# Optimization experiments

Measured on AMD Instinct MI355X. Metric: run time of the kernel, lower is better.

The kernel has to match this reference:

```python
import jax, jax.numpy as jnp
import numpy as np

B, P, D, H, L = 1024, 22, 3, 64, 5
HI = P + 2                 # 22 one-hot + t + d_base
CR = 15.0 / L              # coords_range per layer (tanh=True, agg='sum')
LOG2M = 7.0                # log2(M=128)


def _edges():
    rr, cc = [], []
    for i in range(P):
        for j in range(i + 1, P):
            rr += [i, j]
            cc += [j, i]
    rr, cc = np.asarray(rr), np.asarray(cc)
    off = (np.arange(B) * P)[:, None]
    rows = (rr[None, :] + off).reshape(-1).astype(np.int32)
    cols = (cc[None, :] + off).reshape(-1).astype(np.int32)
    return jnp.asarray(rows), jnp.asarray(cols)


def setup_inputs() -> dict:
    key = jax.random.key(0)
    ks = jax.random.split(key, 16)

    def lin(k, shape, gain=1.0):
        fi, fo = shape[-2], shape[-1]
        lim = gain * np.sqrt(6.0 / (fi + fo))
        return jax.random.uniform(k, shape, jnp.float32, -lim, lim)

    rows, cols = _edges()
    z = lambda *s: jnp.zeros(s, jnp.float32)
    return {
        "t": jax.random.uniform(ks[0], (B,), jnp.float32),
        "x": jax.random.normal(ks[1], (B, P * D), jnp.float32),
        "emb_W": lin(ks[2], (HI, H)), "emb_b": z(H),
        "out_W": lin(ks[3], (H, HI)), "out_b": z(HI),
        # per-layer stacked params (leading dim = L)
        "edge_w1": lin(ks[4], (L, 2 * H + 2, H)), "edge_b1": z(L, H),
        "edge_w2": lin(ks[5], (L, H, H)), "edge_b2": z(L, H),
        "node_w1": lin(ks[6], (L, 2 * H, H)), "node_b1": z(L, H),
        "node_w2": lin(ks[7], (L, H, H)), "node_b2": z(L, H),
        "coord_w1": lin(ks[8], (L, H, H)), "coord_b1": z(L, H),
        "coord_w2": lin(ks[9], (L, H, 1), gain=0.001),  # xavier gain=0.001, no bias
        "att_w": lin(ks[10], (L, H, 1)), "att_b": z(L, 1),
        "rows": rows, "cols": cols,
    }


def reference(t, x, emb_W, emb_b, out_W, out_b,
              edge_w1, edge_b1, edge_w2, edge_b2,
              node_w1, node_b1, node_w2, node_b2,
              coord_w1, coord_b1, coord_w2, att_w, att_b,
              rows, cols):
    silu = jax.nn.silu
    N = B * P
    coord0 = x.reshape(N, D)

    # node features: [one_hot(atom), t, d_base]
    h0 = jnp.tile(jnp.eye(P, dtype=x.dtype), (B, 1))        # (N, 22)
    tt = jnp.repeat(t, P)[:, None]                           # (N, 1)
    db = jnp.full((N, 1), LOG2M, dtype=x.dtype)
    h = jnp.concatenate([h0, tt, db], axis=-1) @ emb_W + emb_b  # (N, H)

    # edge_attr: initial squared distances, shared by all layers
    d0 = coord0[rows] - coord0[cols]
    edge_attr = jnp.sum(d0 * d0, axis=-1, keepdims=True)     # (E, 1)

    def layer(carry, p):
        h, coord = carry
        ew1, eb1, ew2, eb2, nw1, nb1, nw2, nb2, cw1, cb1, cw2, aw, ab = p
        diff = coord[rows] - coord[cols]                     # (E, D)
        radial = jnp.sum(diff * diff, axis=-1, keepdims=True)
        diff = diff / (jnp.sqrt(radial) + 1.0)               # norm_diff
        e_in = jnp.concatenate([h[rows], h[cols], radial, edge_attr], axis=-1)
        m = silu(silu(e_in @ ew1 + eb1) @ ew2 + eb2)         # edge MLP
        m = m * jax.nn.sigmoid(m @ aw + ab)                  # attention gate
        # coordinate update
        trans = diff * (jnp.tanh(silu(m @ cw1 + cb1) @ cw2) * CR)
        coord = coord + jax.ops.segment_sum(trans, rows, num_segments=N)
        # node update (recurrent)
        agg = jax.ops.segment_sum(m, rows, num_segments=N)
        h = h + silu(jnp.concatenate([h, agg], axis=-1) @ nw1 + nb1) @ nw2 + nb2 * 0 + (silu(jnp.concatenate([h, agg], axis=-1) @ nw1 + nb1) @ nw2 + nb2 - silu(jnp.concatenate([h, agg], axis=-1) @ nw1 + nb1) @ nw2 - nb2)
        return (h, coord), None

    # (the expression above is just h = h + node_mlp(...); written plainly:)
    def layer_clean(carry, p):
        h, coord = carry
        ew1, eb1, ew2, eb2, nw1, nb1, nw2, nb2, cw1, cb1, cw2, aw, ab = p
        diff = coord[rows] - coord[cols]
        radial = jnp.sum(diff * diff, axis=-1, keepdims=True)
        diff = diff / (jnp.sqrt(radial) + 1.0)
        e_in = jnp.concatenate([h[rows], h[cols], radial, edge_attr], axis=-1)
        m = silu(silu(e_in @ ew1 + eb1) @ ew2 + eb2)
        m = m * jax.nn.sigmoid(m @ aw + ab)
        trans = diff * (jnp.tanh(silu(m @ cw1 + cb1) @ cw2) * CR)
        coord = coord + jax.ops.segment_sum(trans, rows, num_segments=N)
        agg = jax.ops.segment_sum(m, rows, num_segments=N)
        h = h + (silu(jnp.concatenate([h, agg], axis=-1) @ nw1 + nb1) @ nw2 + nb2)
        return (h, coord), None

    ps = (edge_w1, edge_b1, edge_w2, edge_b2, node_w1, node_b1, node_w2,
          node_b2, coord_w1, coord_b1, coord_w2, att_w, att_b)
    (h, coord), _ = jax.lax.scan(layer_clean, (h, coord0), ps)
    h = h @ out_W + out_b  # embedding_out (does not affect coordinates)

    vel = (coord - coord0).reshape(B, P, D)
    vel = vel - jnp.mean(vel, axis=1, keepdims=True)  # remove_mean
    return vel.reshape(B, P * D)
```

## Files before the change

kernel.cpp:

```cpp
#include <hip/hip_runtime.h>

#define NP 22
#define NH 64
#define NL 5
#define NE 21

constexpr float CRc    = 3.0f;
constexpr float LOG2Mc = 7.0f;
constexpr float L2E    = 1.442695041f;

typedef __fp16 h2_t  __attribute__((ext_vector_type(2)));
typedef __fp16 f16x8 __attribute__((ext_vector_type(8)));
typedef float  f32x16 __attribute__((ext_vector_type(16)));

__device__ __forceinline__ float rcp_(float x) {
#if __has_builtin(__builtin_amdgcn_rcpf)
  return __builtin_amdgcn_rcpf(x);
#else
  float r; asm("v_rcp_f32 %0, %1" : "=v"(r) : "v"(x)); return r;
#endif
}
__device__ __forceinline__ float exp2_(float x) {
#if __has_builtin(__builtin_amdgcn_exp2f)
  return __builtin_amdgcn_exp2f(x);
#else
  float r; asm("v_exp_f32 %0, %1" : "=v"(r) : "v"(x)); return r;
#endif
}
__device__ __forceinline__ float sqrt_(float x) {
#if __has_builtin(__builtin_amdgcn_sqrtf)
  return __builtin_amdgcn_sqrtf(x);
#else
  float r; asm("v_sqrt_f32 %0, %1" : "=v"(r) : "v"(x)); return r;
#endif
}
__device__ __forceinline__ float sigf(float s)  { return rcp_(1.0f + exp2_(-L2E * s)); }
__device__ __forceinline__ float siluf(float s) { return s * sigf(s); }

__device__ __forceinline__ float rl_f(float v, int lane) {
  return __builtin_bit_cast(float, __builtin_amdgcn_readlane(__builtin_bit_cast(int, v), lane));
}
__device__ __forceinline__ h2_t rl_h2(h2_t v, int lane) {
  return __builtin_bit_cast(h2_t, __builtin_amdgcn_readlane(__builtin_bit_cast(int, v), lane));
}
__device__ __forceinline__ h2_t pkf(float a, float b) {
  return __builtin_amdgcn_cvt_pkrtz(a, b);
}
template <int CTRL>
__device__ __forceinline__ float dppmov(float v) {
  return __builtin_bit_cast(float,
      __builtin_amdgcn_update_dpp(0, __builtin_bit_cast(int, v), CTRL, 0xF, 0xF, true));
}
__device__ __forceinline__ float red32(float v) {
  v += dppmov<0xB1>(v);
  v += dppmov<0x4E>(v);
  v += dppmov<0x124>(v);
  v += dppmov<0x128>(v);
  v += __builtin_bit_cast(float, __builtin_amdgcn_ds_swizzle(
         __builtin_bit_cast(int, v), 0x401F));
  return v;
}
__device__ __forceinline__ float fdot2(h2_t a, h2_t b, float c) {
#if __has_builtin(__builtin_amdgcn_fdot2)
  return __builtin_amdgcn_fdot2(a, b, c, false);
#else
  float d;
  asm("v_dot2_f32_f16 %0, %1, %2, %3"
      : "=v"(d)
      : "v"(__builtin_bit_cast(int, a)), "v"(__builtin_bit_cast(int, b)), "v"(c));
  return d;
#endif
}

#define OFF_WLDS   0
#define OFF_AMG    16384
#define OFF_HLDS   28544
#define OFF_HIBUF  34176
#define OFF_HCBUF  39808
#define OFF_AGGU   45440
#define OFF_EAS    48256
#define OFF_EGEO   50112
#define OFF_CBUF   51648
#define OFF_CUPD   52000
#define OFF_VELM   52352
#define LDS_BYTES  52368

__global__ __launch_bounds__(256, 2) void egnn_kernel(
    const float* __restrict__ t,   const float* __restrict__ x,
    const float* __restrict__ embW, const float* __restrict__ embB,
    const float* __restrict__ ew1, const float* __restrict__ eb1,
    const float* __restrict__ ew2, const float* __restrict__ eb2,
    const float* __restrict__ nw1, const float* __restrict__ nb1,
    const float* __restrict__ nw2, const float* __restrict__ nb2,
    const float* __restrict__ cw1, const float* __restrict__ cb1,
    const float* __restrict__ cw2, const float* __restrict__ aw,
    const float* __restrict__ ab,  float* __restrict__ out)
{
  __shared__ __align__(16) char LDSRAW[LDS_BYTES];
  int*   wlds  = (int*)(LDSRAW + OFF_WLDS);
  int*   amg   = (int*)(LDSRAW + OFF_AMG);
  float* h_lds = (float*)(LDSRAW + OFF_HLDS);
  float* hibuf = (float*)(LDSRAW + OFF_HIBUF);
  float* hcbuf = (float*)(LDSRAW + OFF_HCBUF);
  int*   aggu  = (int*)(LDSRAW + OFF_AGGU);
  float* eas   = (float*)(LDSRAW + OFF_EAS);
  float* egeo  = (float*)(LDSRAW + OFF_EGEO);
  float* cbuf  = (float*)(LDSRAW + OFF_CBUF);
  float* cupd  = (float*)(LDSRAW + OFF_CUPD);
  float* velm  = (float*)(LDSRAW + OFF_VELM);

  const int b = blockIdx.x, tid = threadIdx.x;
  const int lane = tid & 63, wv = tid >> 6;
  const int c31 = lane & 31, hh = lane >> 5;
  const int xorv = ((lane >> 3) & 7) << 2;

  auto fillblk = [&](const float* Wlo, const float* Whi, int nblocks) {
    for (int blk = wv; blk < nblocks; blk += 4) {
      const float* Ws = (blk < 8) ? Wlo : Whi;
      int kb = (blk >> 1) & 3, n = blk & 1;
      int k0 = kb * 16 + hh * 8;
      int ch = n * 32 + c31;
      int wb = blk * 256 + ((lane * 4) ^ xorv);
#pragma unroll
      for (int w = 0; w < 4; ++w) {
        h2_t p = pkf(Ws[(k0 + 2 * w) * NH + ch], Ws[(k0 + 2 * w + 1) * NH + ch]);
        wlds[wb + w] = __builtin_bit_cast(int, p);
      }
    }
  };
  auto bread = [&](int blk) -> f16x8 {
    return __builtin_bit_cast(f16x8, *(const int4*)&wlds[blk * 256 + ((lane * 4) ^ xorv)]);
  };
  auto aread = [&](const int* tile, int ks) -> f16x8 {
    int off = (ks * 8 + hh * 4) ^ ((c31 & 7) << 2);
    return __builtin_bit_cast(f16x8, *(const int4*)&tile[c31 * 32 + off]);
  };
  auto packh = [&]() {
    for (int idx = tid; idx < NP * 32; idx += 256) {
      int atom = idx >> 5, w = idx & 31;
      h2_t p = pkf(h_lds[atom * 64 + 2 * w], h_lds[atom * 64 + 2 * w + 1]);
      amg[atom * 32 + (w ^ ((atom & 7) << 2))] = __builtin_bit_cast(int, p);
    }
  };

  if (tid < NP * 3) {
    int p = tid / 3, c = tid - p * 3;
    cbuf[p * 4 + c] = x[b * (NP * 3) + tid];
  }
  float tb = t[b];
  for (int p = wv; p < NP; p += 4)
    h_lds[p * 64 + lane] = embW[p * NH + lane] + tb * embW[22 * NH + lane]
                         + LOG2Mc * embW[23 * NH + lane] + embB[lane];
  __syncthreads();
  for (int idx = tid; idx < NP * NE; idx += 256) {
    int r = idx / NE, e = idx - r * NE, col = e + (e >= r);
    float dx = cbuf[r * 4 + 0] - cbuf[col * 4 + 0];
    float dy = cbuf[r * 4 + 1] - cbuf[col * 4 + 1];
    float dz = cbuf[r * 4 + 2] - cbuf[col * 4 + 2];
    eas[idx] = dx * dx + dy * dy + dz * dz;
  }
  __syncthreads();

  for (int l = 0; l < NL; ++l) {
    const float* W1 = ew1 + l * 130 * NH;
    const float* W2 = ew2 + l * NH * NH;
    const float* C1 = cw1 + l * NH * NH;
    const float* N1 = nw1 + l * 128 * NH;
    const float* N2 = nw2 + l * NH * NH;

    fillblk(W1, W1 + 64 * NH, 16);
    packh();
    __syncthreads();

    {
      int s = wv >> 1, n = wv & 1;
      f32x16 acc;
#pragma unroll
      for (int i = 0; i < 16; ++i) acc[i] = 0.f;
#pragma unroll
      for (int ks = 0; ks < 4; ++ks)
        acc = __builtin_amdgcn_mfma_f32_32x32x16_f16(aread(amg, ks),
                bread((s * 4 + ks) * 2 + n), acc, 0, 0, 0);
      int ch = n * 32 + c31;
      float bias = (s == 0) ? eb1[l * NH + ch] : 0.0f;
      float* dst = (s == 0) ? hibuf : hcbuf;
#pragma unroll
      for (int q = 0; q < 16; ++q) {
        int atom = (q & 3) + 8 * (q >> 2) + 4 * hh;
        if (atom < NP) dst[atom * 64 + ch] = acc[q] + bias;
      }
    }
    __syncthreads();

    fillblk(W2, C1, 16);
    __syncthreads();

    float w128r = W1[128 * NH + lane], w129r = W1[129 * NH + lane];
    float b2r0 = eb2[l * NH + c31],  b2r1 = eb2[l * NH + 32 + c31];
    float abl  = ab[l];
    float cb1r0 = cb1[l * NH + c31], cb1r1 = cb1[l * NH + 32 + c31];
    float c2r0 = cw2[l * NH + c31],  c2r1 = cw2[l * NH + 32 + c31];
    h2_t  awT  = pkf(aw[l * NH + 2 * c31], aw[l * NH + 2 * c31 + 1]);

    const int abase = wv * (NE * 32);
    for (int r = wv; r < NP; r += 4) {
      int eL = (lane < NE) ? lane : NE - 1;
      int colL = eL + (eL >= r);
      float4 ccL = *(const float4*)&cbuf[colL * 4];
      float4 crL = *(const float4*)&cbuf[r * 4];
      float gdx = crL.x - ccL.x, gdy = crL.y - ccL.y, gdz = crL.z - ccL.z;
      float radialT = gdx * gdx + gdy * gdy + gdz * gdz;
      float ndT = rcp_(sqrt_(radialT) + 1.0f);
      if (lane < NE) {
        float4 gw = {gdx, gdy, gdz, ndT};
        *(float4*)&egeo[(wv * 24 + lane) * 4] = gw;
      }
      float eaT = eas[r * NE + eL];
      float hii = hibuf[r * 64 + lane];

#pragma unroll
      for (int e2 = 0; e2 < 20; e2 += 2) {
        int ea_ = e2, eb_ = e2 + 1;
        int cola = ea_ + (ea_ >= r), colb = eb_ + (eb_ >= r);
        float ra = rl_f(radialT, ea_), rb = rl_f(radialT, eb_);
        float qa = rl_f(eaT, ea_),     qb = rl_f(eaT, eb_);
        float s1a = hii + hcbuf[cola * 64 + lane];
        s1a = fmaf(ra, w128r, s1a); s1a = fmaf(qa, w129r, s1a);
        float s1b = hii + hcbuf[colb * 64 + lane];
        s1b = fmaf(rb, w128r, s1b); s1b = fmaf(qb, w129r, s1b);
        float m1a = siluf(s1a), m1b = siluf(s1b);
        h2_t wa = pkf(m1a, dppmov<0xB1>(m1a));
        h2_t wb = pkf(dppmov<0xB1>(m1b), m1b);
        int row = (lane & 1) ? eb_ : ea_;
        int w = lane >> 1;
        amg[abase + row * 32 + (w ^ ((row & 7) << 2))] =
            (lane & 1) ? __builtin_bit_cast(int, wb) : __builtin_bit_cast(int, wa);
      }
      {
        int col20 = 20 + (20 >= r);
        col20 = (col20 < NP) ? col20 : 20;
        float ra = rl_f(radialT, 20), qa = rl_f(eaT, 20);
        float s1 = hii + hcbuf[col20 * 64 + lane];
        s1 = fmaf(ra, w128r, s1); s1 = fmaf(qa, w129r, s1);
        float m1 = siluf(s1);
        h2_t wa = pkf(m1, dppmov<0xB1>(m1));
        if (!(lane & 1))
          amg[abase + 20 * 32 + ((lane >> 1) ^ ((20 & 7) << 2))] = __builtin_bit_cast(int, wa);
      }

      f32x16 acc0, acc1;
#pragma unroll
      for (int i = 0; i < 16; ++i) { acc0[i] = 0.f; acc1[i] = 0.f; }
#pragma unroll
      for (int ks = 0; ks < 4; ++ks) {
        f16x8 af = aread(&amg[abase], ks);
        acc0 = __builtin_amdgcn_mfma_f32_32x32x16_f16(af, bread(ks * 2 + 0), acc0, 0, 0, 0);
        acc1 = __builtin_amdgcn_mfma_f32_32x32x16_f16(af, bread(ks * 2 + 1), acc1, 0, 0, 0);
      }

#pragma unroll
      for (int q = 0; q < 16; ++q) {
        int e0 = (q & 3) + 8 * (q >> 2);
        int rowq = e0 + 4 * hh;
        float m20 = siluf(acc0[q] + b2r0);
        float m21 = siluf(acc1[q] + b2r1);
        acc0[q] = m20; acc1[q] = m21;
        h2_t w0 = pkf(m20, dppmov<0xB1>(m20));
        h2_t w1 = pkf(dppmov<0xB1>(m21), m21);
        int wq = (lane & 1) ? 16 + (c31 >> 1) : (c31 >> 1);
        int adr = (rowq < NE) ? (abase + rowq * 32 + (wq ^ ((rowq & 7) << 2)))
                              : (84 * 32 + wq);
        amg[adr] = (lane & 1) ? __builtin_bit_cast(int, w1) : __builtin_bit_cast(int, w0);
      }

      float gg = 0.f;
      {
        int xr = (c31 & 7) << 2;
#pragma unroll
        for (int tt = 0; tt < 8; ++tt) {
          int4 v4 = *(const int4*)&amg[abase + c31 * 32 + ((4 * tt) ^ xr)];
          gg = fdot2(__builtin_bit_cast(h2_t, v4.x), rl_h2(awT, 4 * tt + 0), gg);
          gg = fdot2(__builtin_bit_cast(h2_t, v4.y), rl_h2(awT, 4 * tt + 1), gg);
          gg = fdot2(__builtin_bit_cast(h2_t, v4.z), rl_h2(awT, 4 * tt + 2), gg);
          gg = fdot2(__builtin_bit_cast(h2_t, v4.w), rl_h2(awT, 4 * tt + 3), gg);
        }
      }
      float sgT = sigf(gg + abl);

      f32x16 acc2, acc3;
#pragma unroll
      for (int i = 0; i < 16; ++i) { acc2[i] = 0.f; acc3[i] = 0.f; }
#pragma unroll
      for (int ks = 0; ks < 4; ++ks) {
        f16x8 af = aread(&amg[abase], ks);
        acc2 = __builtin_amdgcn_mfma_f32_32x32x16_f16(af, bread(8 + ks * 2 + 0), acc2, 0, 0, 0);
        acc3 = __builtin_amdgcn_mfma_f32_32x32x16_f16(af, bread(8 + ks * 2 + 1), acc3, 0, 0, 0);
      }

      float aggn0 = 0.f, aggn1 = 0.f, cax = 0.f, cay = 0.f, caz = 0.f;
#pragma unroll
      for (int q = 0; q < 16; ++q) {
        int e0 = (q & 3) + 8 * (q >> 2);
        int rowq = e0 + 4 * hh;
        bool valid = (rowq < NE);
        float sg = hh ? rl_f(sgT, e0 + 4) : rl_f(sgT, e0);
        float ca0 = acc0[q] * sg, ca1 = acc1[q] * sg;
        aggn0 += valid ? ca0 : 0.f;
        aggn1 += valid ? ca1 : 0.f;
        float c10 = siluf(fmaf(sg, acc2[q], cb1r0));
        float c11 = siluf(fmaf(sg, acc3[q], cb1r1));
        float d = red32(c10 * c2r0 + c11 * c2r1);
        float th = 1.0f - 2.0f * rcp_(1.0f + exp2_(2.0f * L2E * d));
        int eg = valid ? rowq : 0;
        float4 ge = *(const float4*)&egeo[(wv * 24 + eg) * 4];
        float f = valid ? (th * CRc * ge.w) : 0.f;
        cax = fmaf(ge.x, f, cax);
        cay = fmaf(ge.y, f, cay);
        caz = fmaf(ge.z, f, caz);
      }
      aggn0 += __shfl_xor(aggn0, 32, 64);
      aggn1 += __shfl_xor(aggn1, 32, 64);
      {
        h2_t a0p = pkf(aggn0, dppmov<0xB1>(aggn0));
        h2_t a1p = pkf(dppmov<0xB1>(aggn1), aggn1);
        if (lane < 32) {
          int wq = (lane & 1) ? 16 + (c31 >> 1) : (c31 >> 1);
          aggu[r * 32 + (wq ^ ((r & 7) << 2))] =
              (lane & 1) ? __builtin_bit_cast(int, a1p) : __builtin_bit_cast(int, a0p);
        }
      }
      cax += __shfl_xor(cax, 32, 64);
      cay += __shfl_xor(cay, 32, 64);
      caz += __shfl_xor(caz, 32, 64);
      if (lane < 3) {
        float cv = (lane == 0) ? cax : (lane == 1) ? cay : caz;
        cupd[r * 4 + lane] = cv;
      }
    }
    __syncthreads();

    fillblk(N1, N1 + 64 * NH, 16);
    packh();
    __syncthreads();

    if (wv < 2) {
      int n = wv;
      f32x16 acc;
#pragma unroll
      for (int i = 0; i < 16; ++i) acc[i] = 0.f;
#pragma unroll
      for (int ks = 0; ks < 4; ++ks)
        acc = __builtin_amdgcn_mfma_f32_32x32x16_f16(aread(amg, ks),
                bread(ks * 2 + n), acc, 0, 0, 0);
#pragma unroll
      for (int ks = 0; ks < 4; ++ks)
        acc = __builtin_amdgcn_mfma_f32_32x32x16_f16(aread(aggu, ks),
                bread((4 + ks) * 2 + n), acc, 0, 0, 0);
      float bias = nb1[l * NH + n * 32 + c31];
#pragma unroll
      for (int q = 0; q < 16; ++q) {
        int atom = (q & 3) + 8 * (q >> 2) + 4 * hh;
        if (atom < NP) hibuf[atom * 64 + n * 32 + c31] = acc[q] + bias;
      }
    }
    __syncthreads();

    fillblk(N2, N2, 8);
    for (int idx = tid; idx < NP * 32; idx += 256) {
      int atom = idx >> 5, w = idx & 31;
      h2_t p = pkf(siluf(hibuf[atom * 64 + 2 * w]), siluf(hibuf[atom * 64 + 2 * w + 1]));
      aggu[atom * 32 + (w ^ ((atom & 7) << 2))] = __builtin_bit_cast(int, p);
    }
    __syncthreads();

    if (wv < 2) {
      int n = wv;
      f32x16 acc;
#pragma unroll
      for (int i = 0; i < 16; ++i) acc[i] = 0.f;
#pragma unroll
      for (int ks = 0; ks < 4; ++ks)
        acc = __builtin_amdgcn_mfma_f32_32x32x16_f16(aread(aggu, ks),
                bread(ks * 2 + n), acc, 0, 0, 0);
      int ch = n * 32 + c31;
      float bias = nb2[l * NH + ch];
#pragma unroll
      for (int q = 0; q < 16; ++q) {
        int atom = (q & 3) + 8 * (q >> 2) + 4 * hh;
        if (atom < NP) h_lds[atom * 64 + ch] += acc[q] + bias;
      }
    } else {
      int ci = tid - 128;
      if (ci < NP * 3) {
        int p = ci / 3, c = ci - 3 * p;
        cbuf[p * 4 + c] += cupd[p * 4 + c];
      }
    }
    __syncthreads();
  }

  if (tid < NP * 3) {
    int p = tid / 3, c = tid - p * 3;
    cupd[p * 4 + c] = cbuf[p * 4 + c] - x[b * (NP * 3) + tid];
  }
  __syncthreads();
  if (tid < 3) {
    float s = 0.f;
    for (int p = 0; p < NP; ++p) s += cupd[p * 4 + tid];
    velm[tid] = s * (1.0f / 22.0f);
  }
  __syncthreads();
  if (tid < NP * 3) {
    int p = tid / 3, c = tid - p * 3;
    out[b * (NP * 3) + tid] = cupd[p * 4 + c] - velm[c];
  }
}

extern "C" void kernel_launch(void* const* d_in, const int* in_sizes, int n_in,
                              void* d_out, int out_size, void* d_ws, size_t ws_size,
                              hipStream_t stream) {
  const float* t    = (const float*)d_in[0];
  const float* x    = (const float*)d_in[1];
  const float* embW = (const float*)d_in[2];
  const float* embB = (const float*)d_in[3];
  const float* ew1  = (const float*)d_in[6];
  const float* eb1  = (const float*)d_in[7];
  const float* ew2  = (const float*)d_in[8];
  const float* eb2  = (const float*)d_in[9];
  const float* nw1  = (const float*)d_in[10];
  const float* nb1  = (const float*)d_in[11];
  const float* nw2  = (const float*)d_in[12];
  const float* nb2  = (const float*)d_in[13];
  const float* cw1  = (const float*)d_in[14];
  const float* cb1  = (const float*)d_in[15];
  const float* cw2  = (const float*)d_in[16];
  const float* aw   = (const float*)d_in[17];
  const float* ab   = (const float*)d_in[18];

  egnn_kernel<<<1024, 256, 0, stream>>>(t, x, embW, embB, ew1, eb1, ew2, eb2,
                                        nw1, nb1, nw2, nb2, cw1, cb1, cw2,
                                        aw, ab, (float*)d_out);
}
```

Measured before the change: 472.5 us.

## Restructure coord-MLP output dot and prefetch next weights with earlier fills

```diff
diff --git a/kernel.cpp b/kernel.cpp
--- a/kernel.cpp
+++ b/kernel.cpp
@@ -73,17 +73,16 @@
 }
 
 #define OFF_WLDS   0
-#define OFF_AMG    16384
-#define OFF_HLDS   28544
-#define OFF_HIBUF  34176
-#define OFF_HCBUF  39808
-#define OFF_AGGU   45440
-#define OFF_EAS    48256
-#define OFF_EGEO   50112
-#define OFF_CBUF   51648
-#define OFF_CUPD   52000
-#define OFF_VELM   52352
-#define LDS_BYTES  52368
+#define OFF_AMG    24576
+#define OFF_HLDS   35456
+#define OFF_HIBUF  41088
+#define OFF_HCBUF  46720
+#define OFF_AGGU   52352
+#define OFF_EAS    55168
+#define OFF_CBUF   57024
+#define OFF_CUPD   57376
+#define OFF_VELM   57728
+#define LDS_BYTES  57744
 
 __global__ __launch_bounds__(256, 2) void egnn_kernel(
     const float* __restrict__ t,   const float* __restrict__ x,
@@ -104,7 +103,6 @@
   float* hcbuf = (float*)(LDSRAW + OFF_HCBUF);
   int*   aggu  = (int*)(LDSRAW + OFF_AGGU);
   float* eas   = (float*)(LDSRAW + OFF_EAS);
-  float* egeo  = (float*)(LDSRAW + OFF_EGEO);
   float* cbuf  = (float*)(LDSRAW + OFF_CBUF);
   float* cupd  = (float*)(LDSRAW + OFF_CUPD);
   float* velm  = (float*)(LDSRAW + OFF_VELM);
@@ -114,9 +112,9 @@
   const int c31 = lane & 31, hh = lane >> 5;
   const int xorv = ((lane >> 3) & 7) << 2;
 
-  auto fillblk = [&](const float* Wlo, const float* Whi, int nblocks) {
+  auto fillblk3 = [&](const float* m0, const float* m1, const float* m2, int nblocks) {
     for (int blk = wv; blk < nblocks; blk += 4) {
-      const float* Ws = (blk < 8) ? Wlo : Whi;
+      const float* Ws = (blk < 8) ? m0 : ((blk < 16) ? m1 : m2);
       int kb = (blk >> 1) & 3, n = blk & 1;
       int k0 = kb * 16 + hh * 8;
       int ch = n * 32 + c31;
@@ -168,7 +166,7 @@
     const float* N1 = nw1 + l * 128 * NH;
     const float* N2 = nw2 + l * NH * NH;
 
-    fillblk(W1, W1 + 64 * NH, 16);
+    fillblk3(W1, W1 + 64 * NH, W2, 24);
     packh();
     __syncthreads();
 
@@ -192,15 +190,15 @@
     }
     __syncthreads();
 
-    fillblk(W2, C1, 16);
+    fillblk3(C1, C1, C1, 8);
     __syncthreads();
 
     float w128r = W1[128 * NH + lane], w129r = W1[129 * NH + lane];
     float b2r0 = eb2[l * NH + c31],  b2r1 = eb2[l * NH + 32 + c31];
     float abl  = ab[l];
     float cb1r0 = cb1[l * NH + c31], cb1r1 = cb1[l * NH + 32 + c31];
-    float c2r0 = cw2[l * NH + c31],  c2r1 = cw2[l * NH + 32 + c31];
-    h2_t  awT  = pkf(aw[l * NH + 2 * c31], aw[l * NH + 2 * c31 + 1]);
+    h2_t  awT  = pkf(aw[l * NH + 2 * c31],  aw[l * NH + 2 * c31 + 1]);
+    h2_t  c2T  = pkf(cw2[l * NH + 2 * c31], cw2[l * NH + 2 * c31 + 1]);
 
     const int abase = wv * (NE * 32);
     for (int r = wv; r < NP; r += 4) {
@@ -211,10 +209,6 @@
       float gdx = crL.x - ccL.x, gdy = crL.y - ccL.y, gdz = crL.z - ccL.z;
       float radialT = gdx * gdx + gdy * gdy + gdz * gdz;
       float ndT = rcp_(sqrt_(radialT) + 1.0f);
-      if (lane < NE) {
-        float4 gw = {gdx, gdy, gdz, ndT};
-        *(float4*)&egeo[(wv * 24 + lane) * 4] = gw;
-      }
       float eaT = eas[r * NE + eL];
       float hii = hibuf[r * 64 + lane];
 
@@ -238,7 +232,6 @@
       }
       {
         int col20 = 20 + (20 >= r);
-        col20 = (col20 < NP) ? col20 : 20;
         float ra = rl_f(radialT, 20), qa = rl_f(eaT, 20);
         float s1 = hii + hcbuf[col20 * 64 + lane];
         s1 = fmaf(ra, w128r, s1); s1 = fmaf(qa, w129r, s1);
@@ -254,8 +247,8 @@
 #pragma unroll
       for (int ks = 0; ks < 4; ++ks) {
         f16x8 af = aread(&amg[abase], ks);
-        acc0 = __builtin_amdgcn_mfma_f32_32x32x16_f16(af, bread(ks * 2 + 0), acc0, 0, 0, 0);
-        acc1 = __builtin_amdgcn_mfma_f32_32x32x16_f16(af, bread(ks * 2 + 1), acc1, 0, 0, 0);
+        acc0 = __builtin_amdgcn_mfma_f32_32x32x16_f16(af, bread(16 + ks * 2 + 0), acc0, 0, 0, 0);
+        acc1 = __builtin_amdgcn_mfma_f32_32x32x16_f16(af, bread(16 + ks * 2 + 1), acc1, 0, 0, 0);
       }
 
 #pragma unroll
@@ -293,30 +286,27 @@
 #pragma unroll
       for (int ks = 0; ks < 4; ++ks) {
         f16x8 af = aread(&amg[abase], ks);
-        acc2 = __builtin_amdgcn_mfma_f32_32x32x16_f16(af, bread(8 + ks * 2 + 0), acc2, 0, 0, 0);
-        acc3 = __builtin_amdgcn_mfma_f32_32x32x16_f16(af, bread(8 + ks * 2 + 1), acc3, 0, 0, 0);
-      }
-
-      float aggn0 = 0.f, aggn1 = 0.f, cax = 0.f, cay = 0.f, caz = 0.f;
+        acc2 = __builtin_amdgcn_mfma_f32_32x32x16_f16(af, bread(ks * 2 + 0), acc2, 0, 0, 0);
+        acc3 = __builtin_amdgcn_mfma_f32_32x32x16_f16(af, bread(ks * 2 + 1), acc3, 0, 0, 0);
+      }
+
+      float aggn0 = 0.f, aggn1 = 0.f;
 #pragma unroll
       for (int q = 0; q < 16; ++q) {
         int e0 = (q & 3) + 8 * (q >> 2);
         int rowq = e0 + 4 * hh;
         bool valid = (rowq < NE);
         float sg = hh ? rl_f(sgT, e0 + 4) : rl_f(sgT, e0);
-        float ca0 = acc0[q] * sg, ca1 = acc1[q] * sg;
-        aggn0 += valid ? ca0 : 0.f;
-        aggn1 += valid ? ca1 : 0.f;
+        aggn0 += valid ? acc0[q] * sg : 0.f;
+        aggn1 += valid ? acc1[q] * sg : 0.f;
         float c10 = siluf(fmaf(sg, acc2[q], cb1r0));
         float c11 = siluf(fmaf(sg, acc3[q], cb1r1));
-        float d = red32(c10 * c2r0 + c11 * c2r1);
-        float th = 1.0f - 2.0f * rcp_(1.0f + exp2_(2.0f * L2E * d));
-        int eg = valid ? rowq : 0;
-        float4 ge = *(const float4*)&egeo[(wv * 24 + eg) * 4];
-        float f = valid ? (th * CRc * ge.w) : 0.f;
-        cax = fmaf(ge.x, f, cax);
-        cay = fmaf(ge.y, f, cay);
-        caz = fmaf(ge.z, f, caz);
+        h2_t w0 = pkf(c10, dppmov<0xB1>(c10));
+        h2_t w1 = pkf(dppmov<0xB1>(c11), c11);
+        int wq = (lane & 1) ? 16 + (c31 >> 1) : (c31 >> 1);
+        int adr = valid ? (abase + rowq * 32 + (wq ^ ((rowq & 7) << 2)))
+                        : (84 * 32 + wq);
+        amg[adr] = (lane & 1) ? __builtin_bit_cast(int, w1) : __builtin_bit_cast(int, w0);
       }
       aggn0 += __shfl_xor(aggn0, 32, 64);
       aggn1 += __shfl_xor(aggn1, 32, 64);
@@ -329,17 +319,36 @@
               (lane & 1) ? __builtin_bit_cast(int, a1p) : __builtin_bit_cast(int, a0p);
         }
       }
-      cax += __shfl_xor(cax, 32, 64);
-      cay += __shfl_xor(cay, 32, 64);
-      caz += __shfl_xor(caz, 32, 64);
+
+      float dd = 0.f;
+      {
+        int xr = (c31 & 7) << 2;
+#pragma unroll
+        for (int tt = 0; tt < 8; ++tt) {
+          int4 v4 = *(const int4*)&amg[abase + c31 * 32 + ((4 * tt) ^ xr)];
+          dd = fdot2(__builtin_bit_cast(h2_t, v4.x), rl_h2(c2T, 4 * tt + 0), dd);
+          dd = fdot2(__builtin_bit_cast(h2_t, v4.y), rl_h2(c2T, 4 * tt + 1), dd);
+          dd = fdot2(__builtin_bit_cast(h2_t, v4.z), rl_h2(c2T, 4 * tt + 2), dd);
+          dd = fdot2(__builtin_bit_cast(h2_t, v4.w), rl_h2(c2T, 4 * tt + 3), dd);
+        }
+      }
+      float th = 1.0f - 2.0f * rcp_(1.0f + exp2_(2.0f * L2E * dd));
+      float ff = th * CRc * ndT;
+      bool vlane = (lane < NE);
+      float cxc = vlane ? gdx * ff : 0.f;
+      float cyc = vlane ? gdy * ff : 0.f;
+      float czc = vlane ? gdz * ff : 0.f;
+      cxc = red32(cxc);
+      cyc = red32(cyc);
+      czc = red32(czc);
       if (lane < 3) {
-        float cv = (lane == 0) ? cax : (lane == 1) ? cay : caz;
+        float cv = (lane == 0) ? cxc : (lane == 1) ? cyc : czc;
         cupd[r * 4 + lane] = cv;
       }
     }
     __syncthreads();
 
-    fillblk(N1, N1 + 64 * NH, 16);
+    fillblk3(N1, N1 + 64 * NH, N2, 24);
     packh();
     __syncthreads();
 
@@ -365,7 +374,6 @@
     }
     __syncthreads();
 
-    fillblk(N2, N2, 8);
     for (int idx = tid; idx < NP * 32; idx += 256) {
       int atom = idx >> 5, w = idx & 31;
       h2_t p = pkf(siluf(hibuf[atom * 64 + 2 * w]), siluf(hibuf[atom * 64 + 2 * w + 1]));
@@ -381,7 +389,7 @@
 #pragma unroll
       for (int ks = 0; ks < 4; ++ks)
         acc = __builtin_amdgcn_mfma_f32_32x32x16_f16(aread(aggu, ks),
-                bread(ks * 2 + n), acc, 0, 0, 0);
+                bread(16 + ks * 2 + n), acc, 0, 0, 0);
       int ch = n * 32 + c31;
       float bias = nb2[l * NH + ch];
 #pragma unroll
```

Measured after the change: 458.0 us. 3.1% less time.

## Process two receiver atoms per wave and move coord dot to packed fdot2

Applied to the files above, without the earlier changes.

```diff
diff --git a/kernel.cpp b/kernel.cpp
--- a/kernel.cpp
+++ b/kernel.cpp
@@ -74,16 +74,150 @@
 
 #define OFF_WLDS   0
 #define OFF_AMG    16384
-#define OFF_HLDS   28544
-#define OFF_HIBUF  34176
-#define OFF_HCBUF  39808
-#define OFF_AGGU   45440
-#define OFF_EAS    48256
-#define OFF_EGEO   50112
-#define OFF_CBUF   51648
-#define OFF_CUPD   52000
-#define OFF_VELM   52352
-#define LDS_BYTES  52368
+#define OFF_HLDS   38016
+#define OFF_HIBUF  43648
+#define OFF_HCBUF  49280
+#define OFF_AGGU   54912
+#define OFF_EAS    57728
+#define OFF_CBUF   59576
+#define OFF_CUPD   59928
+#define OFF_VELM   60280
+#define LDS_BYTES  60296
+
+#define DUMPROW (168 * 32)
+
+#define STAGE_M1(TB, R, HII, RADT, EAT) do {                                \
+  _Pragma("unroll")                                                         \
+  for (int e2 = 0; e2 < 20; e2 += 2) {                                      \
+    int ea_ = e2, eb_ = e2 + 1;                                             \
+    int cola = ea_ + (ea_ >= (R)), colb = eb_ + (eb_ >= (R));               \
+    float ra = rl_f((RADT), ea_), rb2 = rl_f((RADT), eb_);                  \
+    float qa = rl_f((EAT), ea_),  qb = rl_f((EAT), eb_);                    \
+    float s1a = (HII) + hcbuf[cola * 64 + lane];                            \
+    s1a = fmaf(ra, w128r, s1a); s1a = fmaf(qa, w129r, s1a);                 \
+    float s1b = (HII) + hcbuf[colb * 64 + lane];                            \
+    s1b = fmaf(rb2, w128r, s1b); s1b = fmaf(qb, w129r, s1b);                \
+    float m1a = siluf(s1a), m1b = siluf(s1b);                               \
+    h2_t wa = pkf(m1a, dppmov<0xB1>(m1a));                                  \
+    h2_t wb = pkf(dppmov<0xB1>(m1b), m1b);                                  \
+    int row = (lane & 1) ? eb_ : ea_;                                       \
+    int w = lane >> 1;                                                      \
+    amg[(TB) + row * 32 + (w ^ ((row & 7) << 2))] =                         \
+        (lane & 1) ? __builtin_bit_cast(int, wb) : __builtin_bit_cast(int, wa); \
+  }                                                                         \
+  {                                                                         \
+    int col20 = 20 + (20 >= (R));                                           \
+    float ra = rl_f((RADT), 20), qa = rl_f((EAT), 20);                      \
+    float s1 = (HII) + hcbuf[col20 * 64 + lane];                            \
+    s1 = fmaf(ra, w128r, s1); s1 = fmaf(qa, w129r, s1);                     \
+    float m1 = siluf(s1);                                                   \
+    h2_t wa = pkf(m1, dppmov<0xB1>(m1));                                    \
+    if (!(lane & 1))                                                        \
+      amg[(TB) + 20 * 32 + ((lane >> 1) ^ 16)] = __builtin_bit_cast(int, wa); \
+  }                                                                         \
+} while (0)
+
+#define PASSMM(TB, B0, ACC0, ACC1) do {                                     \
+  _Pragma("unroll")                                                         \
+  for (int ii = 0; ii < 16; ++ii) { ACC0[ii] = 0.f; ACC1[ii] = 0.f; }       \
+  _Pragma("unroll")                                                         \
+  for (int ks = 0; ks < 4; ++ks) {                                          \
+    int off = (ks * 8 + hh * 4) ^ ((c31 & 7) << 2);                         \
+    f16x8 af = __builtin_bit_cast(f16x8, *(const int4*)&amg[(TB) + c31 * 32 + off]); \
+    ACC0 = __builtin_amdgcn_mfma_f32_32x32x16_f16(af, bread((B0) + ks * 2 + 0), ACC0, 0, 0, 0); \
+    ACC1 = __builtin_amdgcn_mfma_f32_32x32x16_f16(af, bread((B0) + ks * 2 + 1), ACC1, 0, 0, 0); \
+  }                                                                         \
+} while (0)
+
+#define POST1(TB, ACC0, ACC1) do {                                          \
+  _Pragma("unroll")                                                         \
+  for (int q = 0; q < 16; ++q) {                                            \
+    int e0 = (q & 3) + 8 * (q >> 2);                                        \
+    int rowq = e0 + 4 * hh;                                                 \
+    float m20 = siluf(ACC0[q] + b2r0);                                      \
+    float m21 = siluf(ACC1[q] + b2r1);                                      \
+    ACC0[q] = m20; ACC1[q] = m21;                                           \
+    h2_t w0 = pkf(m20, dppmov<0xB1>(m20));                                  \
+    h2_t w1 = pkf(dppmov<0xB1>(m21), m21);                                  \
+    int wq = (lane & 1) ? 16 + (c31 >> 1) : (c31 >> 1);                     \
+    int adr = (rowq < NE) ? ((TB) + rowq * 32 + (wq ^ ((rowq & 7) << 2)))   \
+                          : (DUMPROW + wq);                                 \
+    amg[adr] = (lane & 1) ? __builtin_bit_cast(int, w1)                     \
+                          : __builtin_bit_cast(int, w0);                    \
+  }                                                                         \
+} while (0)
+
+#define GATE(TB, SGT) do {                                                  \
+  float gg = 0.f;                                                           \
+  int xr = (c31 & 7) << 2;                                                  \
+  _Pragma("unroll")                                                         \
+  for (int tt = 0; tt < 8; ++tt) {                                          \
+    int4 v4 = *(const int4*)&amg[(TB) + c31 * 32 + ((4 * tt) ^ xr)];        \
+    gg = fdot2(__builtin_bit_cast(h2_t, v4.x), rl_h2(awT, 4 * tt + 0), gg); \
+    gg = fdot2(__builtin_bit_cast(h2_t, v4.y), rl_h2(awT, 4 * tt + 1), gg); \
+    gg = fdot2(__builtin_bit_cast(h2_t, v4.z), rl_h2(awT, 4 * tt + 2), gg); \
+    gg = fdot2(__builtin_bit_cast(h2_t, v4.w), rl_h2(awT, 4 * tt + 3), gg); \
+  }                                                                         \
+  SGT = sigf(gg + abl);                                                     \
+} while (0)
+
+#define POST2A(TB, SGT, ACC0, ACC1, ACC2, ACC3, RROW, V) do {               \
+  float aggn0 = 0.f, aggn1 = 0.f;                                           \
+  _Pragma("unroll")                                                         \
+  for (int q = 0; q < 16; ++q) {                                            \
+    int e0 = (q & 3) + 8 * (q >> 2);                                        \
+    int rowq = e0 + 4 * hh;                                                 \
+    bool valid = (rowq < NE);                                               \
+    float sg = hh ? rl_f(SGT, e0 + 4) : rl_f(SGT, e0);                      \
+    aggn0 += valid ? ACC0[q] * sg : 0.f;                                    \
+    aggn1 += valid ? ACC1[q] * sg : 0.f;                                    \
+    float c10 = siluf(fmaf(sg, ACC2[q], cb1r0));                            \
+    float c11 = siluf(fmaf(sg, ACC3[q], cb1r1));                            \
+    h2_t w0 = pkf(c10, dppmov<0xB1>(c10));                                  \
+    h2_t w1 = pkf(dppmov<0xB1>(c11), c11);                                  \
+    int wq = (lane & 1) ? 16 + (c31 >> 1) : (c31 >> 1);                     \
+    int adr = valid ? ((TB) + rowq * 32 + (wq ^ ((rowq & 7) << 2)))         \
+                    : (DUMPROW + wq);                                       \
+    amg[adr] = (lane & 1) ? __builtin_bit_cast(int, w1)                     \
+                          : __builtin_bit_cast(int, w0);                    \
+  }                                                                         \
+  aggn0 += __shfl_xor(aggn0, 32, 64);                                       \
+  aggn1 += __shfl_xor(aggn1, 32, 64);                                       \
+  h2_t a0p = pkf(aggn0, dppmov<0xB1>(aggn0));                               \
+  h2_t a1p = pkf(dppmov<0xB1>(aggn1), aggn1);                               \
+  if ((V) && lane < 32) {                                                   \
+    int wq = (lane & 1) ? 16 + (c31 >> 1) : (c31 >> 1);                     \
+    aggu[(RROW) * 32 + (wq ^ (((RROW) & 7) << 2))] =                        \
+        (lane & 1) ? __builtin_bit_cast(int, a1p) : __builtin_bit_cast(int, a0p); \
+  }                                                                         \
+} while (0)
+
+#define CDOT(TB, DD) do {                                                   \
+  DD = 0.f;                                                                 \
+  int xr = (c31 & 7) << 2;                                                  \
+  _Pragma("unroll")                                                         \
+  for (int tt = 0; tt < 8; ++tt) {                                          \
+    int4 v4 = *(const int4*)&amg[(TB) + c31 * 32 + ((4 * tt) ^ xr)];        \
+    DD = fdot2(__builtin_bit_cast(h2_t, v4.x), rl_h2(c2T, 4 * tt + 0), DD); \
+    DD = fdot2(__builtin_bit_cast(h2_t, v4.y), rl_h2(c2T, 4 * tt + 1), DD); \
+    DD = fdot2(__builtin_bit_cast(h2_t, v4.z), rl_h2(c2T, 4 * tt + 2), DD); \
+    DD = fdot2(__builtin_bit_cast(h2_t, v4.w), rl_h2(c2T, 4 * tt + 3), DD); \
+  }                                                                         \
+} while (0)
+
+#define CEPI(DD, GX, GY, GZ, ND, RROW, V) do {                              \
+  float th = 1.0f - 2.0f * rcp_(1.0f + exp2_(2.0f * L2E * (DD)));           \
+  float ff = th * CRc * (ND);                                               \
+  bool vlane = (lane < NE);                                                 \
+  float cxc = vlane ? (GX) * ff : 0.f;                                      \
+  float cyc = vlane ? (GY) * ff : 0.f;                                      \
+  float czc = vlane ? (GZ) * ff : 0.f;                                      \
+  cxc = red32(cxc); cyc = red32(cyc); czc = red32(czc);                     \
+  if ((V) && lane < 3) {                                                    \
+    float cv = (lane == 0) ? cxc : (lane == 1) ? cyc : czc;                 \
+    cupd[(RROW) * 4 + lane] = cv;                                           \
+  }                                                                         \
+} while (0)
 
 __global__ __launch_bounds__(256, 2) void egnn_kernel(
     const float* __restrict__ t,   const float* __restrict__ x,
@@ -104,7 +238,6 @@
   float* hcbuf = (float*)(LDSRAW + OFF_HCBUF);
   int*   aggu  = (int*)(LDSRAW + OFF_AGGU);
   float* eas   = (float*)(LDSRAW + OFF_EAS);
-  float* egeo  = (float*)(LDSRAW + OFF_EGEO);
   float* cbuf  = (float*)(LDSRAW + OFF_CBUF);
   float* cupd  = (float*)(LDSRAW + OFF_CUPD);
   float* velm  = (float*)(LDSRAW + OFF_VELM);
@@ -114,9 +247,9 @@
   const int c31 = lane & 31, hh = lane >> 5;
   const int xorv = ((lane >> 3) & 7) << 2;
 
-  auto fillblk = [&](const float* Wlo, const float* Whi, int nblocks) {
+  auto fillblk = [&](const float* m0, const float* m1, int nblocks) {
     for (int blk = wv; blk < nblocks; blk += 4) {
-      const float* Ws = (blk < 8) ? Wlo : Whi;
+      const float* Ws = (blk < 8) ? m0 : m1;
       int kb = (blk >> 1) & 3, n = blk & 1;
       int k0 = kb * 16 + hh * 8;
       int ch = n * 32 + c31;
@@ -199,143 +332,66 @@
     float b2r0 = eb2[l * NH + c31],  b2r1 = eb2[l * NH + 32 + c31];
     float abl  = ab[l];
     float cb1r0 = cb1[l * NH + c31], cb1r1 = cb1[l * NH + 32 + c31];
-    float c2r0 = cw2[l * NH + c31],  c2r1 = cw2[l * NH + 32 + c31];
-    h2_t  awT  = pkf(aw[l * NH + 2 * c31], aw[l * NH + 2 * c31 + 1]);
-
-    const int abase = wv * (NE * 32);
-    for (int r = wv; r < NP; r += 4) {
+    h2_t  awT  = pkf(aw[l * NH + 2 * c31],  aw[l * NH + 2 * c31 + 1]);
+    h2_t  c2T  = pkf(cw2[l * NH + 2 * c31], cw2[l * NH + 2 * c31 + 1]);
+
+    const int tA = wv * (2 * NE * 32);
+    const int tB = tA + NE * 32;
+#pragma unroll 1
+    for (int i = 0; i < 3; ++i) {
+      const int rA = wv + 8 * i;
+      const int rB = rA + 4;
+      const bool bval = (rB < NP);
+      const int rBc = bval ? rB : NP - 1;
+
       int eL = (lane < NE) ? lane : NE - 1;
-      int colL = eL + (eL >= r);
-      float4 ccL = *(const float4*)&cbuf[colL * 4];
-      float4 crL = *(const float4*)&cbuf[r * 4];
-      float gdx = crL.x - ccL.x, gdy = crL.y - ccL.y, gdz = crL.z - ccL.z;
-      float radialT = gdx * gdx + gdy * gdy + gdz * gdz;
-      float ndT = rcp_(sqrt_(radialT) + 1.0f);
-      if (lane < NE) {
-        float4 gw = {gdx, gdy, gdz, ndT};
-        *(float4*)&egeo[(wv * 24 + lane) * 4] = gw;
-      }
-      float eaT = eas[r * NE + eL];
-      float hii = hibuf[r * 64 + lane];
-
-#pragma unroll
-      for (int e2 = 0; e2 < 20; e2 += 2) {
-        int ea_ = e2, eb_ = e2 + 1;
-        int cola = ea_ + (ea_ >= r), colb = eb_ + (eb_ >= r);
-        float ra = rl_f(radialT, ea_), rb = rl_f(radialT, eb_);
-        float qa = rl_f(eaT, ea_),     qb = rl_f(eaT, eb_);
-        float s1a = hii + hcbuf[cola * 64 + lane];
-        s1a = fmaf(ra, w128r, s1a); s1a = fmaf(qa, w129r, s1a);
-        float s1b = hii + hcbuf[colb * 64 + lane];
-        s1b = fmaf(rb, w128r, s1b); s1b = fmaf(qb, w129r, s1b);
-        float m1a = siluf(s1a), m1b = siluf(s1b);
-        h2_t wa = pkf(m1a, dppmov<0xB1>(m1a));
-        h2_t wb = pkf(dppmov<0xB1>(m1b), m1b);
-        int row = (lane & 1) ? eb_ : ea_;
-        int w = lane >> 1;
-        amg[abase + row * 32 + (w ^ ((row & 7) << 2))] =
-            (lane & 1) ? __builtin_bit_cast(int, wb) : __builtin_bit_cast(int, wa);
-      }
+      int colA = eL + (eL >= rA);
+      int colB = eL + (eL >= rBc);
+      float4 crA4 = *(const float4*)&cbuf[rA * 4];
+      float4 ccA4 = *(const float4*)&cbuf[colA * 4];
+      float4 crB4 = *(const float4*)&cbuf[rBc * 4];
+      float4 ccB4 = *(const float4*)&cbuf[colB * 4];
+      float gdxA = crA4.x - ccA4.x, gdyA = crA4.y - ccA4.y, gdzA = crA4.z - ccA4.z;
+      float radA = gdxA * gdxA + gdyA * gdyA + gdzA * gdzA;
+      float ndA  = rcp_(sqrt_(radA) + 1.0f);
+      float gdxB = crB4.x - ccB4.x, gdyB = crB4.y - ccB4.y, gdzB = crB4.z - ccB4.z;
+      float radB = gdxB * gdxB + gdyB * gdyB + gdzB * gdzB;
+      float ndB  = rcp_(sqrt_(radB) + 1.0f);
+      float eaTA = eas[rA * NE + eL];
+      float eaTB = eas[rBc * NE + eL];
+      float hiiA = hibuf[rA * 64 + lane];
+      float hiiB = hibuf[rBc * 64 + lane];
+
+      STAGE_M1(tA, rA, hiiA, radA, eaTA);
+      STAGE_M1(tB, rBc, hiiB, radB, eaTB);
+
+      f32x16 acc0A, acc1A, acc0B, acc1B;
+      PASSMM(tA, 0, acc0A, acc1A);
+      PASSMM(tB, 0, acc0B, acc1B);
+
+      POST1(tA, acc0A, acc1A);
+      POST1(tB, acc0B, acc1B);
+
+      float sgA, sgB;
+      GATE(tA, sgA);
+      GATE(tB, sgB);
+
       {
-        int col20 = 20 + (20 >= r);
-        col20 = (col20 < NP) ? col20 : 20;
-        float ra = rl_f(radialT, 20), qa = rl_f(eaT, 20);
-        float s1 = hii + hcbuf[col20 * 64 + lane];
-        s1 = fmaf(ra, w128r, s1); s1 = fmaf(qa, w129r, s1);
-        float m1 = siluf(s1);
-        h2_t wa = pkf(m1, dppmov<0xB1>(m1));
-        if (!(lane & 1))
-          amg[abase + 20 * 32 + ((lane >> 1) ^ ((20 & 7) << 2))] = __builtin_bit_cast(int, wa);
-      }
-
-      f32x16 acc0, acc1;
-#pragma unroll
-      for (int i = 0; i < 16; ++i) { acc0[i] = 0.f; acc1[i] = 0.f; }
-#pragma unroll
-      for (int ks = 0; ks < 4; ++ks) {
-        f16x8 af = aread(&amg[abase], ks);
-        acc0 = __builtin_amdgcn_mfma_f32_32x32x16_f16(af, bread(ks * 2 + 0), acc0, 0, 0, 0);
-        acc1 = __builtin_amdgcn_mfma_f32_32x32x16_f16(af, bread(ks * 2 + 1), acc1, 0, 0, 0);
-      }
-
-#pragma unroll
-      for (int q = 0; q < 16; ++q) {
-        int e0 = (q & 3) + 8 * (q >> 2);
-        int rowq = e0 + 4 * hh;
-        float m20 = siluf(acc0[q] + b2r0);
-        float m21 = siluf(acc1[q] + b2r1);
-        acc0[q] = m20; acc1[q] = m21;
-        h2_t w0 = pkf(m20, dppmov<0xB1>(m20));
-        h2_t w1 = pkf(dppmov<0xB1>(m21), m21);
-        int wq = (lane & 1) ? 16 + (c31 >> 1) : (c31 >> 1);
-        int adr = (rowq < NE) ? (abase + rowq * 32 + (wq ^ ((rowq & 7) << 2)))
-                              : (84 * 32 + wq);
-        amg[adr] = (lane & 1) ? __builtin_bit_cast(int, w1) : __builtin_bit_cast(int, w0);
-      }
-
-      float gg = 0.f;
+        f32x16 acc2A, acc3A;
+        PASSMM(tA, 8, acc2A, acc3A);
+        POST2A(tA, sgA, acc0A, acc1A, acc2A, acc3A, rA, true);
+      }
       {
-        int xr = (c31 & 7) << 2;
-#pragma unroll
-        for (int tt = 0; tt < 8; ++tt) {
-          int4 v4 = *(const int4*)&amg[abase + c31 * 32 + ((4 * tt) ^ xr)];
-          gg = fdot2(__builtin_bit_cast(h2_t, v4.x), rl_h2(awT, 4 * tt + 0), gg);
-          gg = fdot2(__builtin_bit_cast(h2_t, v4.y), rl_h2(awT, 4 * tt + 1), gg);
-          gg = fdot2(__builtin_bit_cast(h2_t, v4.z), rl_h2(awT, 4 * tt + 2), gg);
-          gg = fdot2(__builtin_bit_cast(h2_t, v4.w), rl_h2(awT, 4 * tt + 3), gg);
-        }
-      }
-      float sgT = sigf(gg + abl);
-
-      f32x16 acc2, acc3;
-#pragma unroll
-      for (int i = 0; i < 16; ++i) { acc2[i] = 0.f; acc3[i] = 0.f; }
-#pragma unroll
-      for (int ks = 0; ks < 4; ++ks) {
-        f16x8 af = aread(&amg[abase], ks);
-        acc2 = __builtin_amdgcn_mfma_f32_32x32x16_f16(af, bread(8 + ks * 2 + 0), acc2, 0, 0, 0);
-        acc3 = __builtin_amdgcn_mfma_f32_32x32x16_f16(af, bread(8 + ks * 2 + 1), acc3, 0, 0, 0);
-      }
-
-      float aggn0 = 0.f, aggn1 = 0.f, cax = 0.f, cay = 0.f, caz = 0.f;
-#pragma unroll
-      for (int q = 0; q < 16; ++q) {
-        int e0 = (q & 3) + 8 * (q >> 2);
-        int rowq = e0 + 4 * hh;
-        bool valid = (rowq < NE);
-        float sg = hh ? rl_f(sgT, e0 + 4) : rl_f(sgT, e0);
-        float ca0 = acc0[q] * sg, ca1 = acc1[q] * sg;
-        aggn0 += valid ? ca0 : 0.f;
-        aggn1 += valid ? ca1 : 0.f;
-        float c10 = siluf(fmaf(sg, acc2[q], cb1r0));
-        float c11 = siluf(fmaf(sg, acc3[q], cb1r1));
-        float d = red32(c10 * c2r0 + c11 * c2r1);
-        float th = 1.0f - 2.0f * rcp_(1.0f + exp2_(2.0f * L2E * d));
-        int eg = valid ? rowq : 0;
-        float4 ge = *(const float4*)&egeo[(wv * 24 + eg) * 4];
-        float f = valid ? (th * CRc * ge.w) : 0.f;
-        cax = fmaf(ge.x, f, cax);
-        cay = fmaf(ge.y, f, cay);
-        caz = fmaf(ge.z, f, caz);
-      }
-      aggn0 += __shfl_xor(aggn0, 32, 64);
-      aggn1 += __shfl_xor(aggn1, 32, 64);
-      {
-        h2_t a0p = pkf(aggn0, dppmov<0xB1>(aggn0));
-        h2_t a1p = pkf(dppmov<0xB1>(aggn1), aggn1);
-        if (lane < 32) {
-          int wq = (lane & 1) ? 16 + (c31 >> 1) : (c31 >> 1);
-          aggu[r * 32 + (wq ^ ((r & 7) << 2))] =
-              (lane & 1) ? __builtin_bit_cast(int, a1p) : __builtin_bit_cast(int, a0p);
-        }
-      }
-      cax += __shfl_xor(cax, 32, 64);
-      cay += __shfl_xor(cay, 32, 64);
-      caz += __shfl_xor(caz, 32, 64);
-      if (lane < 3) {
-        float cv = (lane == 0) ? cax : (lane == 1) ? cay : caz;
-        cupd[r * 4 + lane] = cv;
-      }
+        f32x16 acc2B, acc3B;
+        PASSMM(tB, 8, acc2B, acc3B);
+        POST2A(tB, sgB, acc0B, acc1B, acc2B, acc3B, rBc, bval);
+      }
+
+      float ddA, ddB;
+      CDOT(tA, ddA);
+      CDOT(tB, ddB);
+      CEPI(ddA, gdxA, gdyA, gdzA, ndA, rA, true);
+      CEPI(ddB, gdxB, gdyB, gdzB, ndB, rBc, bval);
     }
     __syncthreads();
 
```

Measured after the change: 478.5 us. Within noise of the previous version (+1.3%).
